# Performance work log

Measured on AMD Instinct MI355X. Metric: run time of the kernel, lower is better.

## Reference

```python
import jax, jax.numpy as jnp
import numpy as np

V = 96103   # pegasus-xsum vocab
D = 1024    # d_model
H = 16      # heads
DH = D // H
F = 4096    # ffn
L = 2       # enc and dec layers (reduced from 16 for the reference)
S = 512     # source length
T = 80      # max_length
B = 4       # batch of sources
NS = 5      # num_return_sequences
BN = B * NS # decode streams
TOPK = 100
EOS = 1
MINLEN = 7
EMB_SCALE = float(np.sqrt(D))


def ln(x):
    m = jnp.mean(x, -1, keepdims=True)
    v = jnp.mean((x - m) ** 2, -1, keepdims=True)
    return (x - m) * jax.lax.rsqrt(v + 1e-5)


def setup_inputs() -> dict:
    key = jax.random.key(0)
    ks = jax.random.split(key, 16)
    g = lambda k, s: (jax.random.normal(k, s) * 0.02).astype(jnp.float32)
    return {
        "ids": jax.random.randint(ks[0], (B, S), 0, 96000).astype(jnp.int32),
        "mask": jnp.ones((B, S), jnp.int32),
        "E": g(ks[1], (V, D)),
        "pos_e": g(ks[2], (S, D)),
        "pos_d": g(ks[3], (T, D)),
        "enc_attn_in": g(ks[4], (L, D, 3 * D)),
        "enc_attn_out": g(ks[5], (L, D, D)),
        "enc_ffn1": g(ks[6], (L, D, F)),
        "enc_ffn2": g(ks[7], (L, F, D)),
        "dec_sa_in": g(ks[8], (L, D, 3 * D)),
        "dec_sa_out": g(ks[9], (L, D, D)),
        "dec_ca_q": g(ks[10], (L, D, D)),
        "dec_ca_kv": g(ks[11], (L, D, 2 * D)),
        "dec_ca_out": g(ks[12], (L, D, D)),
        "dec_ffn1": g(ks[13], (L, D, F)),
        "dec_ffn2": g(ks[14], (L, F, D)),
    }


def _generate(ids, mask, E, pos_e, pos_d, enc_attn_in, enc_attn_out, enc_ffn1,
              enc_ffn2, dec_sa_in, dec_sa_out, dec_ca_q, dec_ca_kv, dec_ca_out,
              dec_ffn1, dec_ffn2):
    inv = 1.0 / float(np.sqrt(DH))
    # ---------------- encoder ----------------
    x = E[ids] * EMB_SCALE + pos_e[None]                       # [B,S,D]
    bias = (1.0 - mask.astype(jnp.float32))[:, None, None, :] * -1e9  # [B,1,1,S]
    for l in range(L):
        h = ln(x)
        qkv = h @ enc_attn_in[l]
        q = qkv[..., :D].reshape(B, S, H, DH)
        k = qkv[..., D:2 * D].reshape(B, S, H, DH)
        v = qkv[..., 2 * D:].reshape(B, S, H, DH)
        sc = jnp.einsum('bqhd,bkhd->bhqk', q, k) * inv + bias
        a = jnp.einsum('bhqk,bkhd->bqhd', jax.nn.softmax(sc, -1), v).reshape(B, S, D)
        x = x + a @ enc_attn_out[l]
        h = ln(x)
        x = x + jax.nn.gelu(h @ enc_ffn1[l]) @ enc_ffn2[l]
    enc = ln(x)
    # expand to BN = B * num_return_sequences decode streams
    enc_r = jnp.repeat(enc, NS, axis=0)                        # [BN,S,D]
    bias_r = jnp.repeat(bias, NS, axis=0)[:, :, 0, :]          # [BN,1,S]
    # precompute cross-attn K/V per decoder layer
    ckv = jnp.einsum('bsd,lde->lbse', enc_r, dec_ca_kv)        # [L,BN,S,2D]
    cK = ckv[..., :D].reshape(L, BN, S, H, DH)
    cV = ckv[..., D:].reshape(L, BN, S, H, DH)

    key_base = jax.random.key(1234)
    cache_k0 = jnp.zeros((L, BN, T, H, DH), jnp.float32)
    cache_v0 = jnp.zeros((L, BN, T, H, DH), jnp.float32)

    def step(carry, t):
        ck, cv, prev = carry
        x = E[prev] * EMB_SCALE + pos_d[t]                     # [BN,D]
        for l in range(L):
            h = ln(x)
            qkv = h @ dec_sa_in[l]
            q = qkv[:, :D].reshape(BN, H, DH)
            k = qkv[:, D:2 * D].reshape(BN, H, DH)
            v = qkv[:, 2 * D:].reshape(BN, H, DH)
            ck = ck.at[l, :, t].set(k)
            cv = cv.at[l, :, t].set(v)
            sc = jnp.einsum('bhd,bkhd->bhk', q, ck[l]) * inv
            sc = sc + jnp.where(jnp.arange(T) <= t, 0.0, -1e9)
            a = jnp.einsum('bhk,bkhd->bhd', jax.nn.softmax(sc, -1), cv[l]).reshape(BN, D)
            x = x + a @ dec_sa_out[l]
            h = ln(x)
            q2 = (h @ dec_ca_q[l]).reshape(BN, H, DH)
            sc2 = jnp.einsum('bhd,bshd->bhs', q2, cK[l]) * inv + bias_r
            a2 = jnp.einsum('bhs,bshd->bhd', jax.nn.softmax(sc2, -1), cV[l]).reshape(BN, D)
            x = x + a2 @ dec_ca_out[l]
            h = ln(x)
            x = x + jax.nn.gelu(h @ dec_ffn1[l]) @ dec_ffn2[l]
        x = ln(x)
        logits = x @ E.T                                       # [BN,V]
        forbid = (t < MINLEN - 1) & (jnp.arange(V) == EOS)     # min_length: block EOS
        logits = jnp.where(forbid, -1e9, logits)
        topv, topi = jax.lax.top_k(logits, TOPK)               # top_k=100 sampling
        sel = jax.random.categorical(jax.random.fold_in(key_base, t), topv)
        tok = jnp.take_along_axis(topi, sel[:, None], 1)[:, 0]
        lp = jnp.take_along_axis(jax.nn.log_softmax(logits, -1), tok[:, None], 1)[:, 0]
        return (ck, cv, tok), (tok, lp)

    init = (cache_k0, cache_v0, jnp.zeros((BN,), jnp.int32))  # start token = pad(0)
    _, (toks, lps) = jax.lax.scan(step, init, jnp.arange(T))
    return toks.T, lps.T                                       # [BN,T] each


def reference(ids, mask, E, pos_e, pos_d, enc_attn_in, enc_attn_out, enc_ffn1,
              enc_ffn2, dec_sa_in, dec_sa_out, dec_ca_q, dec_ca_kv, dec_ca_out,
              dec_ffn1, dec_ffn2):
    toks, _ = _generate(ids, mask, E, pos_e, pos_d, enc_attn_in, enc_attn_out,
                        enc_ffn1, enc_ffn2, dec_sa_in, dec_sa_out, dec_ca_q,
                        dec_ca_kv, dec_ca_out, dec_ffn1, dec_ffn2)
    # matches the torch module: [batch, num_seq, max_len] token ids
    return toks.reshape(B, NS, T)
```

## Files before the change

kernel.cpp:

```cpp
#include <hip/hip_runtime.h>
#include <cstdint>
#include <cstddef>

#define DEV __device__ __forceinline__

constexpr int V  = 96103;
constexpr int D  = 1024;
constexpr int H  = 16;
constexpr int DH = 64;
constexpr int F  = 4096;
constexpr int NL = 2;
constexpr int S  = 512;
constexpr int T  = 80;
constexpr int B  = 4;
constexpr int NS = 5;
constexpr int BN = 20;
constexpr int KTOP = 100;
constexpr int EOS = 1;


DEV float gelu_f(float x) {
  float x3 = x * x * x;
  float inner = 0.7978845608028654f * (x + 0.044715f * x3);
  float tt = tanhf(inner);
  return x * (0.5f * (1.0f + tt));
}

DEV void tf2x32(unsigned k0, unsigned k1, unsigned& x0, unsigned& x1) {
  unsigned ks2 = k0 ^ k1 ^ 0x1BD11BDAu;
#define TFR(rr) { x0 += x1; x1 = (x1 << rr) | (x1 >> (32 - rr)); x1 ^= x0; }
  x0 += k0; x1 += k1;
  TFR(13) TFR(15) TFR(26) TFR(6)
  x0 += k1;  x1 += ks2 + 1u;
  TFR(17) TFR(29) TFR(16) TFR(24)
  x0 += ks2; x1 += k0 + 2u;
  TFR(13) TFR(15) TFR(26) TFR(6)
  x0 += k0;  x1 += k1 + 3u;
  TFR(17) TFR(29) TFR(16) TFR(24)
  x0 += k1;  x1 += ks2 + 4u;
  TFR(13) TFR(15) TFR(26) TFR(6)
  x0 += ks2; x1 += k0 + 5u;
#undef TFR
}

DEV unsigned long long sort_key(float v, unsigned idx) {
  unsigned bb = __float_as_uint(v);
  bb = (bb & 0x80000000u) ? ~bb : (bb | 0x80000000u);
  return ((unsigned long long)bb << 32) | (unsigned long long)(0xFFFFFFFFu - idx);
}

template<int NWAVE>
DEV void ln_to_lds(const float* __restrict__ x, float* xs, int tid) {
  int w = tid >> 6, lane = tid & 63;
  for (int m = w; m < BN; m += NWAVE) {
    float4 v[4];
    float sum = 0.0f;
#pragma unroll
    for (int j = 0; j < 4; ++j) {
      v[j] = *(const float4*)(x + m * D + j * 256 + lane * 4);
      sum += v[j].x + v[j].y + v[j].z + v[j].w;
    }
#pragma unroll
    for (int o = 32; o > 0; o >>= 1) sum += __shfl_xor(sum, o);
    float mean = sum * (1.0f / 1024.0f);
    float vs = 0.0f;
#pragma unroll
    for (int j = 0; j < 4; ++j) {
      float a = v[j].x - mean, b = v[j].y - mean, c = v[j].z - mean, d = v[j].w - mean;
      vs += a * a + b * b + c * c + d * d;
    }
#pragma unroll
    for (int o = 32; o > 0; o >>= 1) vs += __shfl_xor(vs, o);
    float rsig = 1.0f / sqrtf(vs * (1.0f / 1024.0f) + 1e-5f);
#pragma unroll
    for (int j = 0; j < 4; ++j) {
      float4 ov;
      ov.x = (v[j].x - mean) * rsig; ov.y = (v[j].y - mean) * rsig;
      ov.z = (v[j].z - mean) * rsig; ov.w = (v[j].w - mean) * rsig;
      *(float4*)(xs + m * D + j * 256 + lane * 4) = ov;
    }
  }
}


__global__ __launch_bounds__(256) void embed_enc(const int* __restrict__ ids,
                                                 const float* __restrict__ E,
                                                 const float* __restrict__ pos_e,
                                                 float* __restrict__ xe) {
  int row = blockIdx.x;
  int id = ids[row];
  const float* er = E + (size_t)id * D;
  const float* pr = pos_e + (size_t)(row % S) * D;
  float* xr = xe + (size_t)row * D;
  for (int j = threadIdx.x; j < D; j += 256)
    xr[j] = er[j] * 32.0f + pr[j];
}

__global__ __launch_bounds__(256) void embed_dec(const float* __restrict__ E,
                                                 const float* __restrict__ pos_d,
                                                 const int* __restrict__ toks,
                                                 float* __restrict__ xd, int t) {
  int bn = blockIdx.x;
  int prev = (t == 0) ? 0 : toks[bn * T + (t - 1)];
  const float* er = E + (size_t)prev * D;
  const float* pr = pos_d + (size_t)t * D;
  float* xr = xd + (size_t)bn * D;
  for (int j = threadIdx.x; j < D; j += 256)
    xr[j] = er[j] * 32.0f + pr[j];
}


__global__ __launch_bounds__(256) void ln_kernel(const float* __restrict__ x,
                                                 float* __restrict__ y) {
  __shared__ float red[256];
  __shared__ float sv[2];
  int tid = threadIdx.x;
  const float* xr = x + (size_t)blockIdx.x * D;
  float4 v = *(const float4*)(xr + tid * 4);
  red[tid] = v.x + v.y + v.z + v.w;
  __syncthreads();
  for (int k = 128; k > 0; k >>= 1) { if (tid < k) red[tid] += red[tid + k]; __syncthreads(); }
  if (tid == 0) sv[0] = red[0] * (1.0f / 1024.0f);
  __syncthreads();
  float m = sv[0];
  float dx = v.x - m, dy = v.y - m, dz = v.z - m, dw = v.w - m;
  red[tid] = dx * dx + dy * dy + dz * dz + dw * dw;
  __syncthreads();
  for (int k = 128; k > 0; k >>= 1) { if (tid < k) red[tid] += red[tid + k]; __syncthreads(); }
  if (tid == 0) sv[1] = 1.0f / sqrtf(red[0] * (1.0f / 1024.0f) + 1e-5f);
  __syncthreads();
  float r = sv[1];
  float* yr = y + (size_t)blockIdx.x * D;
  float4 o; o.x = dx * r; o.y = dy * r; o.z = dz * r; o.w = dw * r;
  *(float4*)(yr + tid * 4) = o;
}


template<int EPI>
__global__ __launch_bounds__(256) void gemm128(const float* __restrict__ A,
                                               const float* __restrict__ W,
                                               const float* X, float* C,
                                               int Kd, int Nd) {
  __shared__ __align__(16) float As[8][128];
  __shared__ __align__(16) float Bs[8][128];
  int tid = threadIdx.x;
  int n0 = blockIdx.x * 128, m0 = blockIdx.y * 128;
  int tx = tid & 15, ty = tid >> 4;
  int ar = tid >> 1, ac = (tid & 1) * 4;
  int br = tid >> 5, bc = (tid & 31) * 4;
  float acc[8][8] = {};
  for (int k0 = 0; k0 < Kd; k0 += 8) {
    float4 av = *(const float4*)(A + (size_t)(m0 + ar) * Kd + k0 + ac);
    float4 wv = *(const float4*)(W + (size_t)(k0 + br) * Nd + n0 + bc);
    __syncthreads();
    As[ac + 0][ar] = av.x; As[ac + 1][ar] = av.y;
    As[ac + 2][ar] = av.z; As[ac + 3][ar] = av.w;
    *(float4*)&Bs[br][bc] = wv;
    __syncthreads();
#pragma unroll
    for (int k = 0; k < 8; ++k) {
      float a8[8], b8[8];
      *(float4*)&a8[0] = *(const float4*)&As[k][ty * 8];
      *(float4*)&a8[4] = *(const float4*)&As[k][ty * 8 + 4];
      *(float4*)&b8[0] = *(const float4*)&Bs[k][tx * 8];
      *(float4*)&b8[4] = *(const float4*)&Bs[k][tx * 8 + 4];
#pragma unroll
      for (int i = 0; i < 8; ++i)
#pragma unroll
        for (int j = 0; j < 8; ++j)
          acc[i][j] = fmaf(a8[i], b8[j], acc[i][j]);
    }
  }
#pragma unroll
  for (int i = 0; i < 8; ++i) {
    int m = m0 + ty * 8 + i;
#pragma unroll
    for (int j = 0; j < 8; ++j) {
      int n = n0 + tx * 8 + j;
      float r = acc[i][j];
      size_t off = (size_t)m * Nd + n;
      if (EPI == 1) r = X[off] + r;
      if (EPI == 2) r = gelu_f(r);
      C[off] = r;
    }
  }
}


__global__ __launch_bounds__(256) void enc_attn(const float* __restrict__ qkv,
                                                const int* __restrict__ mask,
                                                float* __restrict__ ab) {
  __shared__ __align__(16) float qv[64];
  __shared__ float sc[512];
  __shared__ float red[256];
  __shared__ float sv[2];
  int tid = threadIdx.x;
  int q = blockIdx.x % S;
  int h = (blockIdx.x / S) % H;
  int b = blockIdx.x / (S * H);
  const float* qrow = qkv + (size_t)(b * S + q) * (3 * D) + h * 64;
  if (tid < 64) qv[tid] = qrow[tid];
  __syncthreads();
  float lmax = -INFINITY;
  for (int k = tid; k < S; k += 256) {
    const float* kr = qkv + (size_t)(b * S + k) * (3 * D) + D + h * 64;
    float dot = 0.0f;
#pragma unroll
    for (int d4 = 0; d4 < 16; ++d4) {
      float4 kk = *(const float4*)(kr + d4 * 4);
      float4 qq = *(const float4*)(qv + d4 * 4);
      dot += qq.x * kk.x + qq.y * kk.y + qq.z * kk.z + qq.w * kk.w;
    }
    float bias = (1.0f - (float)mask[b * S + k]) * -1e9f;
    float val = dot * 0.125f + bias;
    sc[k] = val;
    lmax = fmaxf(lmax, val);
  }
  red[tid] = lmax; __syncthreads();
  for (int k = 128; k > 0; k >>= 1) { if (tid < k) red[tid] = fmaxf(red[tid], red[tid + k]); __syncthreads(); }
  if (tid == 0) sv[0] = red[0];
  __syncthreads();
  float mx = sv[0];
  float lsum = 0.0f;
  for (int k = tid; k < S; k += 256) { float e = expf(sc[k] - mx); sc[k] = e; lsum += e; }
  red[tid] = lsum; __syncthreads();
  for (int k = 128; k > 0; k >>= 1) { if (tid < k) red[tid] += red[tid + k]; __syncthreads(); }
  if (tid == 0) sv[1] = red[0];
  __syncthreads();
  float den = sv[1];
  for (int k = tid; k < S; k += 256) sc[k] = sc[k] / den;
  __syncthreads();
  int d = tid & 63, c = tid >> 6;
  const float* vb = qkv + (size_t)(b * S) * (3 * D) + 2 * D + h * 64 + d;
  float part = 0.0f;
  for (int k = c * 128; k < c * 128 + 128; ++k)
    part = fmaf(sc[k], vb[(size_t)k * (3 * D)], part);
  red[tid] = part; __syncthreads();
  if (tid < 64) {
    float o = red[tid] + red[tid + 64] + red[tid + 128] + red[tid + 192];
    ab[(size_t)(b * S + q) * D + h * 64 + tid] = o;
  }
}


template<int CT, int EPI, bool KV, bool LNIN>
__global__ __launch_bounds__(512) void dec_gemm(const float* __restrict__ x,
                                                const float* __restrict__ W,
                                                const float* Xres, float* Cout,
                                                float* __restrict__ cacheK,
                                                float* __restrict__ cacheV,
                                                int Kd, int Nd, int t, int l) {
  constexpr int KSP = 512 / CT;
  __shared__ float red[CT * 20 * (KSP + 1)];
  __shared__ float redw[CT * (KSP + 1)];
  __shared__ float sab[40];
  int tid = threadIdx.x;
  if constexpr (LNIN) {
    int w = tid >> 6, lane = tid & 63;
    for (int m = w; m < BN; m += 8) {
      const float* xr = x + (size_t)m * 1024 + lane * 16;
      float4 v[4];
      float sum = 0.0f;
#pragma unroll
      for (int j = 0; j < 4; ++j) {
        v[j] = *(const float4*)(xr + j * 4);
        sum += v[j].x + v[j].y + v[j].z + v[j].w;
      }
#pragma unroll
      for (int o = 32; o > 0; o >>= 1) sum += __shfl_xor(sum, o);
      float mean = sum * (1.0f / 1024.0f);
      float vs = 0.0f;
#pragma unroll
      for (int j = 0; j < 4; ++j) {
        float a = v[j].x - mean, b = v[j].y - mean, c2 = v[j].z - mean, d = v[j].w - mean;
        vs += a * a + b * b + c2 * c2 + d * d;
      }
#pragma unroll
      for (int o = 32; o > 0; o >>= 1) vs += __shfl_xor(vs, o);
      float rstd = 1.0f / sqrtf(vs * (1.0f / 1024.0f) + 1e-5f);
      if (lane == 0) { sab[m] = rstd; sab[20 + m] = -mean * rstd; }
    }
    __syncthreads();
  }
  int c = tid % CT, ks = tid / CT;
  int klen = Kd / KSP;
  const float* Wp = W + (size_t)(ks * klen) * Nd + blockIdx.x * CT + c;
  float acc[20] = {};
  float accw = 0.0f;
  for (int kk = 0; kk < klen; kk += 8) {
    float wv[8];
#pragma unroll
    for (int u = 0; u < 8; ++u) wv[u] = Wp[(size_t)u * Nd];
    Wp += (size_t)8 * Nd;
    if constexpr (LNIN) {
      accw += wv[0] + wv[1] + wv[2] + wv[3] + wv[4] + wv[5] + wv[6] + wv[7];
    }
    int kb = ks * klen + kk;
#pragma unroll
    for (int m = 0; m < 20; ++m) {
      float4 x0 = *(const float4*)(x + (size_t)m * Kd + kb);
      float4 x1 = *(const float4*)(x + (size_t)m * Kd + kb + 4);
      float a = acc[m];
      a = fmaf(x0.x, wv[0], a); a = fmaf(x0.y, wv[1], a);
      a = fmaf(x0.z, wv[2], a); a = fmaf(x0.w, wv[3], a);
      a = fmaf(x1.x, wv[4], a); a = fmaf(x1.y, wv[5], a);
      a = fmaf(x1.z, wv[6], a); a = fmaf(x1.w, wv[7], a);
      acc[m] = a;
    }
  }
#pragma unroll
  for (int m = 0; m < 20; ++m) red[(c * 20 + m) * (KSP + 1) + ks] = acc[m];
  if constexpr (LNIN) redw[c * (KSP + 1) + ks] = accw;
  __syncthreads();
  if (tid < CT * 20) {
    int cc = tid % CT, m = tid / CT;
    const float* rp = red + (cc * 20 + m) * (KSP + 1);
    float s = 0.0f;
#pragma unroll
    for (int k2 = 0; k2 < KSP; ++k2) s += rp[k2];
    if constexpr (LNIN) {
      const float* rw = redw + cc * (KSP + 1);
      float sw = 0.0f;
#pragma unroll
      for (int k2 = 0; k2 < KSP; ++k2) sw += rw[k2];
      s = sab[m] * s + sab[20 + m] * sw;
    }
    int ng = blockIdx.x * CT + cc;
    if constexpr (KV) {
      if (ng < D) {
        Cout[(size_t)m * Nd + ng] = s;
      } else if (ng < 2 * D) {
        cacheK[(((size_t)l * BN + m) * T + t) * D + (ng - D)] = s;
      } else {
        cacheV[(((size_t)l * BN + m) * T + t) * D + (ng - 2 * D)] = s;
      }
    } else {
      size_t off = (size_t)m * Nd + ng;
      if (EPI == 1) s = Xres[off] + s;
      if (EPI == 2) s = gelu_f(s);
      Cout[off] = s;
    }
  }
}


__global__ __launch_bounds__(128) void dec_self_attn(const float* __restrict__ qkvd,
                                                     const float* __restrict__ cacheK,
                                                     const float* __restrict__ cacheV,
                                                     float* __restrict__ ad, int t, int l) {
  __shared__ __align__(16) float qv[64];
  __shared__ float sc[96];
  __shared__ float sv[2];
  int tid = threadIdx.x;
  int bn = blockIdx.x >> 4;
  int h = blockIdx.x & 15;
  int n = t + 1;
  if (tid < 64) qv[tid] = qkvd[(size_t)bn * (3 * D) + h * 64 + tid];
  __syncthreads();
  if (tid < n) {
    const float* kr = cacheK + (((size_t)l * BN + bn) * T + tid) * D + h * 64;
    float dot = 0.0f;
#pragma unroll
    for (int d4 = 0; d4 < 16; ++d4) {
      float4 kk = *(const float4*)(kr + d4 * 4);
      float4 qq = *(const float4*)(qv + d4 * 4);
      dot += qq.x * kk.x + qq.y * kk.y + qq.z * kk.z + qq.w * kk.w;
    }
    sc[tid] = dot * 0.125f;
  }
  __syncthreads();
  if (tid == 0) {
    float mx = -INFINITY;
    for (int k = 0; k < n; ++k) mx = fmaxf(mx, sc[k]);
    sv[0] = mx;
  }
  __syncthreads();
  if (tid < n) sc[tid] = expf(sc[tid] - sv[0]);
  __syncthreads();
  if (tid == 0) {
    float s = 0.0f;
    for (int k = 0; k < n; ++k) s += sc[k];
    sv[1] = s;
  }
  __syncthreads();
  if (tid < n) sc[tid] = sc[tid] / sv[1];
  __syncthreads();
  if (tid < 64) {
    const float* vb = cacheV + ((size_t)l * BN + bn) * T * D + h * 64 + tid;
    float o = 0.0f;
    for (int k = 0; k < n; ++k) o = fmaf(sc[k], vb[(size_t)k * D], o);
    ad[(size_t)bn * D + h * 64 + tid] = o;
  }
}


__global__ __launch_bounds__(256) void dec_cross_attn(const float* __restrict__ q2,
                                                      const float* __restrict__ cKV,
                                                      const int* __restrict__ mask,
                                                      float* __restrict__ ad, int l) {
  __shared__ __align__(16) float qv[64];
  __shared__ float sc[512];
  __shared__ float red[256];
  __shared__ float sv[2];
  int tid = threadIdx.x;
  int bn = blockIdx.x >> 4;
  int h = blockIdx.x & 15;
  int b = bn / NS;
  const float* base = cKV + ((size_t)l * B + b) * S * (2 * D);
  if (tid < 64) qv[tid] = q2[(size_t)bn * D + h * 64 + tid];
  __syncthreads();
  float lmax = -INFINITY;
  for (int s = tid; s < S; s += 256) {
    const float* kr = base + (size_t)s * (2 * D) + h * 64;
    float dot = 0.0f;
#pragma unroll
    for (int d4 = 0; d4 < 16; ++d4) {
      float4 kk = *(const float4*)(kr + d4 * 4);
      float4 qq = *(const float4*)(qv + d4 * 4);
      dot += qq.x * kk.x + qq.y * kk.y + qq.z * kk.z + qq.w * kk.w;
    }
    float bias = (1.0f - (float)mask[b * S + s]) * -1e9f;
    float val = dot * 0.125f + bias;
    sc[s] = val;
    lmax = fmaxf(lmax, val);
  }
  red[tid] = lmax; __syncthreads();
  for (int k = 128; k > 0; k >>= 1) { if (tid < k) red[tid] = fmaxf(red[tid], red[tid + k]); __syncthreads(); }
  if (tid == 0) sv[0] = red[0];
  __syncthreads();
  float mx = sv[0];
  float lsum = 0.0f;
  for (int s = tid; s < S; s += 256) { float e = expf(sc[s] - mx); sc[s] = e; lsum += e; }
  red[tid] = lsum; __syncthreads();
  for (int k = 128; k > 0; k >>= 1) { if (tid < k) red[tid] += red[tid + k]; __syncthreads(); }
  if (tid == 0) sv[1] = red[0];
  __syncthreads();
  float den = sv[1];
  for (int s = tid; s < S; s += 256) sc[s] = sc[s] / den;
  __syncthreads();
  int d = tid & 63, c = tid >> 6;
  const float* vb = base + D + h * 64 + d;
  float part = 0.0f;
  for (int s = c * 128; s < c * 128 + 128; ++s)
    part = fmaf(sc[s], vb[(size_t)s * (2 * D)], part);
  red[tid] = part; __syncthreads();
  if (tid < 64) {
    float o = red[tid] + red[tid + 64] + red[tid + 128] + red[tid + 192];
    ad[(size_t)bn * D + h * 64 + tid] = o;
  }
}


__global__ __launch_bounds__(256) void logits_ln(const float* __restrict__ xd,
                                                 const float* __restrict__ E,
                                                 float* __restrict__ logits) {
  __shared__ float xs[20 * 1024];
  int tid = threadIdx.x;
  ln_to_lds<4>(xd, xs, tid);
  __syncthreads();
  int w = tid >> 6, l = tid & 63;
  int mh = (w >> 1) * 10;
  int ns = w & 1;
  int nb = blockIdx.x * 384 + ns * 192 + l;
  int n1 = nb + 64, n2 = nb + 128;
  const float* e0 = E + (size_t)(nb < V ? nb : V - 1) * D;
  const float* e1 = E + (size_t)(n1 < V ? n1 : V - 1) * D;
  const float* e2 = E + (size_t)(n2 < V ? n2 : V - 1) * D;
  const float* xb = xs + mh * 1024;
  float acc[10][3] = {};
  for (int k = 0; k < 1024; k += 4) {
    float4 ea = *(const float4*)(e0 + k);
    float4 eb = *(const float4*)(e1 + k);
    float4 ec = *(const float4*)(e2 + k);
#pragma unroll
    for (int m = 0; m < 10; ++m) {
      const float4 xv = *(const float4*)(xb + m * 1024 + k);
      float a0 = acc[m][0], a1 = acc[m][1], a2 = acc[m][2];
      a0 = fmaf(xv.x, ea.x, a0); a0 = fmaf(xv.y, ea.y, a0);
      a0 = fmaf(xv.z, ea.z, a0); a0 = fmaf(xv.w, ea.w, a0);
      a1 = fmaf(xv.x, eb.x, a1); a1 = fmaf(xv.y, eb.y, a1);
      a1 = fmaf(xv.z, eb.z, a1); a1 = fmaf(xv.w, eb.w, a1);
      a2 = fmaf(xv.x, ec.x, a2); a2 = fmaf(xv.y, ec.y, a2);
      a2 = fmaf(xv.z, ec.z, a2); a2 = fmaf(xv.w, ec.w, a2);
      acc[m][0] = a0; acc[m][1] = a1; acc[m][2] = a2;
    }
  }
#pragma unroll
  for (int m = 0; m < 10; ++m) {
    if (nb < V) logits[(size_t)(mh + m) * V + nb] = acc[m][0];
    if (n1 < V) logits[(size_t)(mh + m) * V + n1] = acc[m][1];
    if (n2 < V) logits[(size_t)(mh + m) * V + n2] = acc[m][2];
  }
}


__global__ __launch_bounds__(256) void topk_sample(const float* __restrict__ logits,
                                                   int* __restrict__ toks, int t) {
  __shared__ unsigned long long keys[2048];
  __shared__ float svals[128];
  __shared__ unsigned sidx[128];
  int tid = threadIdx.x;
  int bn = blockIdx.x;
  const float* row = logits + (size_t)bn * V;

  float tv[8]; unsigned ti[8];
#pragma unroll
  for (int j = 0; j < 8; ++j) { tv[j] = -INFINITY; ti[j] = 0xFFFFFFFFu; }

  for (int i = tid; i < V; i += 256) {
    float v = row[i];
    if (t < 6 && i == EOS) v = -1e9f;
    if (v > tv[7]) {
      tv[7] = v; ti[7] = (unsigned)i;
#pragma unroll
      for (int j = 7; j > 0; --j) {
        if (tv[j] > tv[j - 1]) {
          float a = tv[j]; tv[j] = tv[j - 1]; tv[j - 1] = a;
          unsigned bi = ti[j]; ti[j] = ti[j - 1]; ti[j - 1] = bi;
        }
      }
    }
  }
#pragma unroll
  for (int j = 0; j < 8; ++j) keys[tid * 8 + j] = ~sort_key(tv[j], ti[j]);
  __syncthreads();

  for (int ksz = 2; ksz <= 2048; ksz <<= 1) {
    for (int jj = ksz >> 1; jj > 0; jj >>= 1) {
      for (int i = tid; i < 2048; i += 256) {
        int ixj = i ^ jj;
        if (ixj > i) {
          unsigned long long a = keys[i], b2 = keys[ixj];
          bool up = ((i & ksz) == 0);
          if ((a > b2) == up) { keys[i] = b2; keys[ixj] = a; }
        }
      }
      __syncthreads();
    }
  }

  if (tid < KTOP) {
    unsigned long long kk = ~keys[tid];
    unsigned sb = (unsigned)(kk >> 32);
    unsigned idx = 0xFFFFFFFFu - (unsigned)(kk & 0xFFFFFFFFull);
    unsigned fb = (sb & 0x80000000u) ? (sb ^ 0x80000000u) : ~sb;
    float v = __uint_as_float(fb);
    unsigned a0 = 0u, a1 = (unsigned)t;
    tf2x32(0u, 1234u, a0, a1);
    unsigned c0 = 0u, c1 = (unsigned)(bn * KTOP + tid);
    tf2x32(a0, a1, c0, c1);
    unsigned bits = c0 ^ c1;
    float f = __uint_as_float((bits >> 9) | 0x3f800000u) - 1.0f;
    float u = fmaxf(f, 1.17549435e-38f);
    float g = -logf(-logf(u));
    svals[tid] = v + g;
    sidx[tid] = idx;
  }
  __syncthreads();
  if (tid == 0) {
    int best = 0; float bv = svals[0];
    for (int j = 1; j < KTOP; ++j) { if (svals[j] > bv) { bv = svals[j]; best = j; } }
    toks[bn * T + t] = (int)sidx[best];
  }
}


extern "C" void kernel_launch(void* const* d_in, const int* in_sizes, int n_in,
                              void* d_out, int out_size, void* d_ws, size_t ws_size,
                              hipStream_t stream) {
  (void)in_sizes; (void)n_in; (void)out_size; (void)ws_size;

  const int*   ids   = (const int*)d_in[0];
  const int*   maskp = (const int*)d_in[1];
  const float* E     = (const float*)d_in[2];
  const float* pos_e = (const float*)d_in[3];
  const float* pos_d = (const float*)d_in[4];
  const float* eai   = (const float*)d_in[5];
  const float* eao   = (const float*)d_in[6];
  const float* ef1   = (const float*)d_in[7];
  const float* ef2   = (const float*)d_in[8];
  const float* dsi   = (const float*)d_in[9];
  const float* dso   = (const float*)d_in[10];
  const float* dcq   = (const float*)d_in[11];
  const float* dckv  = (const float*)d_in[12];
  const float* dco   = (const float*)d_in[13];
  const float* df1   = (const float*)d_in[14];
  const float* df2   = (const float*)d_in[15];

  float* ws = (float*)d_ws;
  size_t o = 0;
  auto alloc = [&](size_t n) { size_t r = o; o += (n + 63) & ~(size_t)63; return r; };
  float* cKV    = ws + alloc((size_t)NL * B * S * 2 * D);
  float* cacheK = ws + alloc((size_t)NL * BN * T * D);
  float* cacheV = ws + alloc((size_t)NL * BN * T * D);
  float* xe     = ws + alloc((size_t)B * S * D);
  float* he     = ws + alloc((size_t)B * S * D);
  float* qkvb   = ws + alloc((size_t)B * S * 3 * D);
  float* ab     = ws + alloc((size_t)B * S * D);
  float* ffb    = ws + alloc((size_t)B * S * F);
  float* xd      = qkvb;
  float* q2      = xd + BN * D;
  float* ad      = q2 + BN * D;
  float* qkvd    = ad + BN * D;
  float* ffd     = qkvd + BN * 3 * D;
  float* logitsb = ffd + BN * F;
  int* toks = (int*)d_out;

  embed_enc<<<B * S, 256, 0, stream>>>(ids, E, pos_e, xe);
  for (int l = 0; l < NL; ++l) {
    ln_kernel<<<B * S, 256, 0, stream>>>(xe, he);
    gemm128<0><<<dim3(3 * D / 128, B * S / 128), 256, 0, stream>>>(
        he, eai + (size_t)l * D * 3 * D, nullptr, qkvb, D, 3 * D);
    enc_attn<<<B * H * S, 256, 0, stream>>>(qkvb, maskp, ab);
    gemm128<1><<<dim3(D / 128, B * S / 128), 256, 0, stream>>>(
        ab, eao + (size_t)l * D * D, xe, xe, D, D);
    ln_kernel<<<B * S, 256, 0, stream>>>(xe, he);
    gemm128<2><<<dim3(F / 128, B * S / 128), 256, 0, stream>>>(
        he, ef1 + (size_t)l * D * F, nullptr, ffb, D, F);
    gemm128<1><<<dim3(D / 128, B * S / 128), 256, 0, stream>>>(
        ffb, ef2 + (size_t)l * F * D, xe, xe, F, D);
  }
  ln_kernel<<<B * S, 256, 0, stream>>>(xe, he);
  for (int l = 0; l < NL; ++l) {
    gemm128<0><<<dim3(2 * D / 128, B * S / 128), 256, 0, stream>>>(
        he, dckv + (size_t)l * D * 2 * D, nullptr,
        cKV + (size_t)l * B * S * 2 * D, D, 2 * D);
  }

  for (int t = 0; t < T; ++t) {
    embed_dec<<<BN, 256, 0, stream>>>(E, pos_d, toks, xd, t);
    for (int l = 0; l < NL; ++l) {
      dec_gemm<16, 0, true, true><<<3 * D / 16, 512, 0, stream>>>(
          xd, dsi + (size_t)l * D * 3 * D, nullptr, qkvd, cacheK, cacheV,
          D, 3 * D, t, l);
      dec_self_attn<<<BN * H, 128, 0, stream>>>(qkvd, cacheK, cacheV, ad, t, l);
      dec_gemm<8, 1, false, false><<<D / 8, 512, 0, stream>>>(
          ad, dso + (size_t)l * D * D, xd, xd, nullptr, nullptr, D, D, 0, 0);
      dec_gemm<8, 0, false, true><<<D / 8, 512, 0, stream>>>(
          xd, dcq + (size_t)l * D * D, nullptr, q2, nullptr, nullptr, D, D, 0, 0);
      dec_cross_attn<<<BN * H, 256, 0, stream>>>(q2, cKV, maskp, ad, l);
      dec_gemm<8, 1, false, false><<<D / 8, 512, 0, stream>>>(
          ad, dco + (size_t)l * D * D, xd, xd, nullptr, nullptr, D, D, 0, 0);
      dec_gemm<16, 2, false, true><<<F / 16, 512, 0, stream>>>(
          xd, df1 + (size_t)l * D * F, nullptr, ffd, nullptr, nullptr, D, F, 0, 0);
      dec_gemm<8, 1, false, false><<<D / 8, 512, 0, stream>>>(
          ffd, df2 + (size_t)l * F * D, xd, xd, nullptr, nullptr, F, D, 0, 0);
    }
    logits_ln<<<(V + 383) / 384, 256, 0, stream>>>(xd, E, logitsb);
    topk_sample<<<BN, 256, 0, stream>>>(logitsb, toks, t);
  }
}
```

Before: 63.65 ms.

## Fold final LayerNorm into logits epilogue and fuse next-token embedding into sampler

The logits kernel stops normalizing all 20 decoder rows into LDS. It computes only per-row mean and rstd, takes raw dot products with the embedding rows plus each embedding row's sum, and applies the affine correction in the epilogue. The tile changes to 192 vocab columns with 5 rows per wave, which doubles the grid, and x is now read from global memory instead of LDS. Separately, the embed_dec launch for the next step moves into the end of topk_sample, saving one kernel launch per step at some risk of precision drift from the algebraic LN folding.

New measurement: 73.11 ms. 1.15x slower.

```diff
diff --git a/kernel.cpp b/kernel.cpp
--- a/kernel.cpp
+++ b/kernel.cpp
@@ -49,39 +49,6 @@
   return ((unsigned long long)bb << 32) | (unsigned long long)(0xFFFFFFFFu - idx);
 }
 
-template<int NWAVE>
-DEV void ln_to_lds(const float* __restrict__ x, float* xs, int tid) {
-  int w = tid >> 6, lane = tid & 63;
-  for (int m = w; m < BN; m += NWAVE) {
-    float4 v[4];
-    float sum = 0.0f;
-#pragma unroll
-    for (int j = 0; j < 4; ++j) {
-      v[j] = *(const float4*)(x + m * D + j * 256 + lane * 4);
-      sum += v[j].x + v[j].y + v[j].z + v[j].w;
-    }
-#pragma unroll
-    for (int o = 32; o > 0; o >>= 1) sum += __shfl_xor(sum, o);
-    float mean = sum * (1.0f / 1024.0f);
-    float vs = 0.0f;
-#pragma unroll
-    for (int j = 0; j < 4; ++j) {
-      float a = v[j].x - mean, b = v[j].y - mean, c = v[j].z - mean, d = v[j].w - mean;
-      vs += a * a + b * b + c * c + d * d;
-    }
-#pragma unroll
-    for (int o = 32; o > 0; o >>= 1) vs += __shfl_xor(vs, o);
-    float rsig = 1.0f / sqrtf(vs * (1.0f / 1024.0f) + 1e-5f);
-#pragma unroll
-    for (int j = 0; j < 4; ++j) {
-      float4 ov;
-      ov.x = (v[j].x - mean) * rsig; ov.y = (v[j].y - mean) * rsig;
-      ov.z = (v[j].z - mean) * rsig; ov.w = (v[j].w - mean) * rsig;
-      *(float4*)(xs + m * D + j * 256 + lane * 4) = ov;
-    }
-  }
-}
-
 
 __global__ __launch_bounds__(256) void embed_enc(const int* __restrict__ ids,
                                                  const float* __restrict__ E,
@@ -292,9 +259,8 @@
 #pragma unroll
     for (int u = 0; u < 8; ++u) wv[u] = Wp[(size_t)u * Nd];
     Wp += (size_t)8 * Nd;
-    if constexpr (LNIN) {
+    if constexpr (LNIN)
       accw += wv[0] + wv[1] + wv[2] + wv[3] + wv[4] + wv[5] + wv[6] + wv[7];
-    }
     int kb = ks * klen + kk;
 #pragma unroll
     for (int m = 0; m < 20; ++m) {
@@ -451,54 +417,92 @@
 }
 
 
-__global__ __launch_bounds__(256) void logits_ln(const float* __restrict__ xd,
-                                                 const float* __restrict__ E,
-                                                 float* __restrict__ logits) {
-  __shared__ float xs[20 * 1024];
-  int tid = threadIdx.x;
-  ln_to_lds<4>(xd, xs, tid);
-  __syncthreads();
-  int w = tid >> 6, l = tid & 63;
-  int mh = (w >> 1) * 10;
-  int ns = w & 1;
-  int nb = blockIdx.x * 384 + ns * 192 + l;
-  int n1 = nb + 64, n2 = nb + 128;
-  const float* e0 = E + (size_t)(nb < V ? nb : V - 1) * D;
+__global__ __launch_bounds__(256) void logits_alg(const float* __restrict__ xd,
+                                                  const float* __restrict__ E,
+                                                  float* __restrict__ logits) {
+  __shared__ float sab[40];
+  int tid = threadIdx.x;
+  int w = tid >> 6, lane = tid & 63;
+  for (int m = w; m < BN; m += 4) {
+    const float* xr = xd + (size_t)m * D + lane * 16;
+    float4 v[4];
+    float sum = 0.0f;
+#pragma unroll
+    for (int j = 0; j < 4; ++j) {
+      v[j] = *(const float4*)(xr + j * 4);
+      sum += v[j].x + v[j].y + v[j].z + v[j].w;
+    }
+#pragma unroll
+    for (int o = 32; o > 0; o >>= 1) sum += __shfl_xor(sum, o);
+    float mean = sum * (1.0f / 1024.0f);
+    float vs = 0.0f;
+#pragma unroll
+    for (int j = 0; j < 4; ++j) {
+      float a = v[j].x - mean, b = v[j].y - mean, c2 = v[j].z - mean, d = v[j].w - mean;
+      vs += a * a + b * b + c2 * c2 + d * d;
+    }
+#pragma unroll
+    for (int o = 32; o > 0; o >>= 1) vs += __shfl_xor(vs, o);
+    float rstd = 1.0f / sqrtf(vs * (1.0f / 1024.0f) + 1e-5f);
+    if (lane == 0) { sab[m] = rstd; sab[20 + m] = -mean * rstd; }
+  }
+  __syncthreads();
+
+  int n0 = blockIdx.x * 192 + lane;
+  int n1 = n0 + 64, n2 = n0 + 128;
+  const float* e0 = E + (size_t)(n0 < V ? n0 : V - 1) * D;
   const float* e1 = E + (size_t)(n1 < V ? n1 : V - 1) * D;
   const float* e2 = E + (size_t)(n2 < V ? n2 : V - 1) * D;
-  const float* xb = xs + mh * 1024;
-  float acc[10][3] = {};
-  for (int k = 0; k < 1024; k += 4) {
-    float4 ea = *(const float4*)(e0 + k);
-    float4 eb = *(const float4*)(e1 + k);
-    float4 ec = *(const float4*)(e2 + k);
-#pragma unroll
-    for (int m = 0; m < 10; ++m) {
-      const float4 xv = *(const float4*)(xb + m * 1024 + k);
+  const float* xb = xd + (size_t)(w * 5) * D;
+  float acc[5][3] = {};
+  float se0 = 0.0f, se1 = 0.0f, se2 = 0.0f;
+  for (int k = 0; k < 1024; k += 8) {
+    float4 ea0 = *(const float4*)(e0 + k), ea1 = *(const float4*)(e0 + k + 4);
+    float4 eb0 = *(const float4*)(e1 + k), eb1 = *(const float4*)(e1 + k + 4);
+    float4 ec0 = *(const float4*)(e2 + k), ec1 = *(const float4*)(e2 + k + 4);
+    se0 += ea0.x + ea0.y + ea0.z + ea0.w + ea1.x + ea1.y + ea1.z + ea1.w;
+    se1 += eb0.x + eb0.y + eb0.z + eb0.w + eb1.x + eb1.y + eb1.z + eb1.w;
+    se2 += ec0.x + ec0.y + ec0.z + ec0.w + ec1.x + ec1.y + ec1.z + ec1.w;
+#pragma unroll
+    for (int m = 0; m < 5; ++m) {
+      float4 x0 = *(const float4*)(xb + (size_t)m * D + k);
+      float4 x1 = *(const float4*)(xb + (size_t)m * D + k + 4);
       float a0 = acc[m][0], a1 = acc[m][1], a2 = acc[m][2];
-      a0 = fmaf(xv.x, ea.x, a0); a0 = fmaf(xv.y, ea.y, a0);
-      a0 = fmaf(xv.z, ea.z, a0); a0 = fmaf(xv.w, ea.w, a0);
-      a1 = fmaf(xv.x, eb.x, a1); a1 = fmaf(xv.y, eb.y, a1);
-      a1 = fmaf(xv.z, eb.z, a1); a1 = fmaf(xv.w, eb.w, a1);
-      a2 = fmaf(xv.x, ec.x, a2); a2 = fmaf(xv.y, ec.y, a2);
-      a2 = fmaf(xv.z, ec.z, a2); a2 = fmaf(xv.w, ec.w, a2);
+      a0 = fmaf(x0.x, ea0.x, a0); a0 = fmaf(x0.y, ea0.y, a0);
+      a0 = fmaf(x0.z, ea0.z, a0); a0 = fmaf(x0.w, ea0.w, a0);
+      a0 = fmaf(x1.x, ea1.x, a0); a0 = fmaf(x1.y, ea1.y, a0);
+      a0 = fmaf(x1.z, ea1.z, a0); a0 = fmaf(x1.w, ea1.w, a0);
+      a1 = fmaf(x0.x, eb0.x, a1); a1 = fmaf(x0.y, eb0.y, a1);
+      a1 = fmaf(x0.z, eb0.z, a1); a1 = fmaf(x0.w, eb0.w, a1);
+      a1 = fmaf(x1.x, eb1.x, a1); a1 = fmaf(x1.y, eb1.y, a1);
+      a1 = fmaf(x1.z, eb1.z, a1); a1 = fmaf(x1.w, eb1.w, a1);
+      a2 = fmaf(x0.x, ec0.x, a2); a2 = fmaf(x0.y, ec0.y, a2);
+      a2 = fmaf(x0.z, ec0.z, a2); a2 = fmaf(x0.w, ec0.w, a2);
+      a2 = fmaf(x1.x, ec1.x, a2); a2 = fmaf(x1.y, ec1.y, a2);
+      a2 = fmaf(x1.z, ec1.z, a2); a2 = fmaf(x1.w, ec1.w, a2);
       acc[m][0] = a0; acc[m][1] = a1; acc[m][2] = a2;
     }
   }
 #pragma unroll
-  for (int m = 0; m < 10; ++m) {
-    if (nb < V) logits[(size_t)(mh + m) * V + nb] = acc[m][0];
-    if (n1 < V) logits[(size_t)(mh + m) * V + n1] = acc[m][1];
-    if (n2 < V) logits[(size_t)(mh + m) * V + n2] = acc[m][2];
+  for (int m = 0; m < 5; ++m) {
+    int row = w * 5 + m;
+    float a = sab[row], b = sab[20 + row];
+    if (n0 < V) logits[(size_t)row * V + n0] = a * acc[m][0] + b * se0;
+    if (n1 < V) logits[(size_t)row * V + n1] = a * acc[m][1] + b * se1;
+    if (n2 < V) logits[(size_t)row * V + n2] = a * acc[m][2] + b * se2;
   }
 }
 
 
 __global__ __launch_bounds__(256) void topk_sample(const float* __restrict__ logits,
-                                                   int* __restrict__ toks, int t) {
+                                                   int* __restrict__ toks,
+                                                   const float* __restrict__ E,
+                                                   const float* __restrict__ pos_d,
+                                                   float* __restrict__ xd, int t) {
   __shared__ unsigned long long keys[2048];
   __shared__ float svals[128];
   __shared__ unsigned sidx[128];
+  __shared__ int stok;
   int tid = threadIdx.x;
   int bn = blockIdx.x;
   const float* row = logits + (size_t)bn * V;
@@ -560,7 +564,17 @@
   if (tid == 0) {
     int best = 0; float bv = svals[0];
     for (int j = 1; j < KTOP; ++j) { if (svals[j] > bv) { bv = svals[j]; best = j; } }
-    toks[bn * T + t] = (int)sidx[best];
+    int tok = (int)sidx[best];
+    toks[bn * T + t] = tok;
+    stok = tok;
+  }
+  __syncthreads();
+  if (t + 1 < T) {
+    int tok = stok;
+    const float* er = E + (size_t)tok * D;
+    const float* pr = pos_d + (size_t)(t + 1) * D;
+    for (int j = tid; j < D; j += 256)
+      xd[(size_t)bn * D + j] = er[j] * 32.0f + pr[j];
   }
 }
 
@@ -627,8 +641,8 @@
         cKV + (size_t)l * B * S * 2 * D, D, 2 * D);
   }
 
+  embed_dec<<<BN, 256, 0, stream>>>(E, pos_d, toks, xd, 0);
   for (int t = 0; t < T; ++t) {
-    embed_dec<<<BN, 256, 0, stream>>>(E, pos_d, toks, xd, t);
     for (int l = 0; l < NL; ++l) {
       dec_gemm<16, 0, true, true><<<3 * D / 16, 512, 0, stream>>>(
           xd, dsi + (size_t)l * D * 3 * D, nullptr, qkvd, cacheK, cacheV,
@@ -646,7 +660,7 @@
       dec_gemm<8, 1, false, false><<<D / 8, 512, 0, stream>>>(
           ffd, df2 + (size_t)l * F * D, xd, xd, nullptr, nullptr, F, D, 0, 0);
     }
-    logits_ln<<<(V + 383) / 384, 256, 0, stream>>>(xd, E, logitsb);
-    topk_sample<<<BN, 256, 0, stream>>>(logitsb, toks, t);
-  }
-}
+    logits_alg<<<(V + 191) / 192, 256, 0, stream>>>(xd, E, logitsb);
+    topk_sample<<<BN, 256, 0, stream>>>(logitsb, toks, E, pos_d, xd, t);
+  }
+}
```

## Restructure logits GEMM per-column, pad vocab rows, fuse next-token embedding into sampling

Applied to the files above, without the earlier changes.

The logits kernel now has each thread own one vocab column and accumulate all 20 decode rows, so every embedding row is read once per block instead of being split across row halves. Logit rows are padded to an even length so top-k can scan them with float4 loads, and the pad slot is filled with a large negative value. The next step's decoder embedding is computed at the end of the sampling kernel, which removes the separate embed launch on every step. Only 188 of 256 threads per block do work in the logits kernel, and each thread keeps a 20-element accumulator, which may raise register pressure.

After: 57.94 ms. -9.0%, faster.

```diff
diff --git a/kernel.cpp b/kernel.cpp
--- a/kernel.cpp
+++ b/kernel.cpp
@@ -5,6 +5,7 @@
 #define DEV __device__ __forceinline__
 
 constexpr int V  = 96103;
+constexpr int VPAD = 96104;
 constexpr int D  = 1024;
 constexpr int H  = 16;
 constexpr int DH = 64;
@@ -17,6 +18,8 @@
 constexpr int BN = 20;
 constexpr int KTOP = 100;
 constexpr int EOS = 1;
+constexpr int LCOLS = 188;
+constexpr int LGRID = (V + LCOLS - 1) / LCOLS;
 
 
 DEV float gelu_f(float x) {
@@ -292,9 +295,8 @@
 #pragma unroll
     for (int u = 0; u < 8; ++u) wv[u] = Wp[(size_t)u * Nd];
     Wp += (size_t)8 * Nd;
-    if constexpr (LNIN) {
+    if constexpr (LNIN)
       accw += wv[0] + wv[1] + wv[2] + wv[3] + wv[4] + wv[5] + wv[6] + wv[7];
-    }
     int kb = ks * klen + kk;
 #pragma unroll
     for (int m = 0; m < 20; ++m) {
@@ -451,72 +453,77 @@
 }
 
 
-__global__ __launch_bounds__(256) void logits_ln(const float* __restrict__ xd,
-                                                 const float* __restrict__ E,
-                                                 float* __restrict__ logits) {
+__global__ __launch_bounds__(256) void logits3(const float* __restrict__ xd,
+                                               const float* __restrict__ E,
+                                               float* __restrict__ logits) {
   __shared__ float xs[20 * 1024];
   int tid = threadIdx.x;
   ln_to_lds<4>(xd, xs, tid);
   __syncthreads();
-  int w = tid >> 6, l = tid & 63;
-  int mh = (w >> 1) * 10;
-  int ns = w & 1;
-  int nb = blockIdx.x * 384 + ns * 192 + l;
-  int n1 = nb + 64, n2 = nb + 128;
-  const float* e0 = E + (size_t)(nb < V ? nb : V - 1) * D;
-  const float* e1 = E + (size_t)(n1 < V ? n1 : V - 1) * D;
-  const float* e2 = E + (size_t)(n2 < V ? n2 : V - 1) * D;
-  const float* xb = xs + mh * 1024;
-  float acc[10][3] = {};
-  for (int k = 0; k < 1024; k += 4) {
-    float4 ea = *(const float4*)(e0 + k);
-    float4 eb = *(const float4*)(e1 + k);
-    float4 ec = *(const float4*)(e2 + k);
-#pragma unroll
-    for (int m = 0; m < 10; ++m) {
-      const float4 xv = *(const float4*)(xb + m * 1024 + k);
-      float a0 = acc[m][0], a1 = acc[m][1], a2 = acc[m][2];
-      a0 = fmaf(xv.x, ea.x, a0); a0 = fmaf(xv.y, ea.y, a0);
-      a0 = fmaf(xv.z, ea.z, a0); a0 = fmaf(xv.w, ea.w, a0);
-      a1 = fmaf(xv.x, eb.x, a1); a1 = fmaf(xv.y, eb.y, a1);
-      a1 = fmaf(xv.z, eb.z, a1); a1 = fmaf(xv.w, eb.w, a1);
-      a2 = fmaf(xv.x, ec.x, a2); a2 = fmaf(xv.y, ec.y, a2);
-      a2 = fmaf(xv.z, ec.z, a2); a2 = fmaf(xv.w, ec.w, a2);
-      acc[m][0] = a0; acc[m][1] = a1; acc[m][2] = a2;
-    }
-  }
-#pragma unroll
-  for (int m = 0; m < 10; ++m) {
-    if (nb < V) logits[(size_t)(mh + m) * V + nb] = acc[m][0];
-    if (n1 < V) logits[(size_t)(mh + m) * V + n1] = acc[m][1];
-    if (n2 < V) logits[(size_t)(mh + m) * V + n2] = acc[m][2];
+  int n = blockIdx.x * LCOLS + tid;
+  if (tid < LCOLS && n < V) {
+    const float* er = E + (size_t)n * D;
+    float acc[20] = {};
+    for (int k = 0; k < 1024; k += 8) {
+      float4 e0 = *(const float4*)(er + k);
+      float4 e1 = *(const float4*)(er + k + 4);
+#pragma unroll
+      for (int m = 0; m < 20; ++m) {
+        const float* xb = xs + m * 1024 + k;
+        float4 x0 = *(const float4*)(xb);
+        float4 x1 = *(const float4*)(xb + 4);
+        float a = acc[m];
+        a = fmaf(x0.x, e0.x, a); a = fmaf(x0.y, e0.y, a);
+        a = fmaf(x0.z, e0.z, a); a = fmaf(x0.w, e0.w, a);
+        a = fmaf(x1.x, e1.x, a); a = fmaf(x1.y, e1.y, a);
+        a = fmaf(x1.z, e1.z, a); a = fmaf(x1.w, e1.w, a);
+        acc[m] = a;
+      }
+    }
+#pragma unroll
+    for (int m = 0; m < 20; ++m)
+      logits[(size_t)m * VPAD + n] = acc[m];
+  } else if (n == V) {
+#pragma unroll
+    for (int m = 0; m < 20; ++m)
+      logits[(size_t)m * VPAD + V] = -1e30f;
   }
 }
 
 
 __global__ __launch_bounds__(256) void topk_sample(const float* __restrict__ logits,
-                                                   int* __restrict__ toks, int t) {
+                                                   int* __restrict__ toks,
+                                                   const float* __restrict__ E,
+                                                   const float* __restrict__ pos_d,
+                                                   float* __restrict__ xd, int t) {
   __shared__ unsigned long long keys[2048];
   __shared__ float svals[128];
   __shared__ unsigned sidx[128];
+  __shared__ int stok;
   int tid = threadIdx.x;
   int bn = blockIdx.x;
-  const float* row = logits + (size_t)bn * V;
+  const float* row = logits + (size_t)bn * VPAD;
 
   float tv[8]; unsigned ti[8];
 #pragma unroll
   for (int j = 0; j < 8; ++j) { tv[j] = -INFINITY; ti[j] = 0xFFFFFFFFu; }
 
-  for (int i = tid; i < V; i += 256) {
-    float v = row[i];
-    if (t < 6 && i == EOS) v = -1e9f;
-    if (v > tv[7]) {
-      tv[7] = v; ti[7] = (unsigned)i;
-#pragma unroll
-      for (int j = 7; j > 0; --j) {
-        if (tv[j] > tv[j - 1]) {
-          float a = tv[j]; tv[j] = tv[j - 1]; tv[j - 1] = a;
-          unsigned bi = ti[j]; ti[j] = ti[j - 1]; ti[j - 1] = bi;
+  for (int i4 = tid * 4; i4 < VPAD; i4 += 1024) {
+    float4 v4 = *(const float4*)(row + i4);
+    float vv[4] = {v4.x, v4.y, v4.z, v4.w};
+#pragma unroll
+    for (int j = 0; j < 4; ++j) {
+      int i = i4 + j;
+      float v = vv[j];
+      if (t < 6 && i == EOS) v = -1e9f;
+      if (v > tv[7]) {
+        tv[7] = v; ti[7] = (unsigned)i;
+#pragma unroll
+        for (int jj = 7; jj > 0; --jj) {
+          if (tv[jj] > tv[jj - 1]) {
+            float a = tv[jj]; tv[jj] = tv[jj - 1]; tv[jj - 1] = a;
+            unsigned bi = ti[jj]; ti[jj] = ti[jj - 1]; ti[jj - 1] = bi;
+          }
         }
       }
     }
@@ -560,7 +567,17 @@
   if (tid == 0) {
     int best = 0; float bv = svals[0];
     for (int j = 1; j < KTOP; ++j) { if (svals[j] > bv) { bv = svals[j]; best = j; } }
-    toks[bn * T + t] = (int)sidx[best];
+    int tok = (int)sidx[best];
+    toks[bn * T + t] = tok;
+    stok = tok;
+  }
+  __syncthreads();
+  if (t + 1 < T) {
+    int tok = stok;
+    const float* er = E + (size_t)tok * D;
+    const float* pr = pos_d + (size_t)(t + 1) * D;
+    for (int j = tid; j < D; j += 256)
+      xd[(size_t)bn * D + j] = er[j] * 32.0f + pr[j];
   }
 }
 
@@ -627,8 +644,8 @@
         cKV + (size_t)l * B * S * 2 * D, D, 2 * D);
   }
 
+  embed_dec<<<BN, 256, 0, stream>>>(E, pos_d, toks, xd, 0);
   for (int t = 0; t < T; ++t) {
-    embed_dec<<<BN, 256, 0, stream>>>(E, pos_d, toks, xd, t);
     for (int l = 0; l < NL; ++l) {
       dec_gemm<16, 0, true, true><<<3 * D / 16, 512, 0, stream>>>(
           xd, dsi + (size_t)l * D * 3 * D, nullptr, qkvd, cacheK, cacheV,
@@ -646,7 +663,7 @@
       dec_gemm<8, 1, false, false><<<D / 8, 512, 0, stream>>>(
           ffd, df2 + (size_t)l * F * D, xd, xd, nullptr, nullptr, F, D, 0, 0);
     }
-    logits_ln<<<(V + 383) / 384, 256, 0, stream>>>(xd, E, logitsb);
-    topk_sample<<<BN, 256, 0, stream>>>(logitsb, toks, t);
-  }
-}
+    logits3<<<LGRID, 256, 0, stream>>>(xd, E, logitsb);
+    topk_sample<<<BN, 256, 0, stream>>>(logitsb, toks, E, pos_d, xd, t);
+  }
+}
```
